# Optimization experiments

Hardware: AMD Instinct MI355X
Metric: run time of the kernel (lower is better)

The kernel has to match this reference:

```python
import jax, jax.numpy as jnp
import numpy as np

N, E, D, H = 100000, 400000, 128, 128  # nodes, edges, feat dim, mlp hidden


def _ln(x, g, b, eps=1e-5):
    m = jnp.mean(x, axis=-1, keepdims=True)
    v = jnp.mean((x - m) ** 2, axis=-1, keepdims=True)
    return (x - m) * jax.lax.rsqrt(v + eps) * g + b


def _mlp(x, w0, b0, w1, b1, w2, b2):
    # Linear->ReLU->Linear->ReLU->Linear (last act = Identity)
    h = jax.nn.relu(x @ w0 + b0)
    h = jax.nn.relu(h @ w1 + b1)
    return h @ w2 + b2


def setup_inputs() -> dict:
    key = jax.random.key(0)
    ks = jax.random.split(key, 16)
    node_x = jax.random.normal(ks[0], (N, D), dtype=jnp.float32)
    edge_attr = jax.random.normal(ks[1], (E, D), dtype=jnp.float32)
    edge_index = jax.random.randint(ks[2], (2, E), 0, N, dtype=jnp.int32)

    def lin(k, fin, fout):
        kw, kb = jax.random.split(k)
        s = 1.0 / np.sqrt(fin)
        w = jax.random.uniform(kw, (fin, fout), jnp.float32, -s, s)
        b = jax.random.uniform(kb, (fout,), jnp.float32, -s, s)
        return w, b

    # message MLP: (3D) -> H -> H -> D, then LayerNorm(D)
    msg_w0, msg_b0 = lin(ks[3], 3 * D, H)
    msg_w1, msg_b1 = lin(ks[4], H, H)
    msg_w2, msg_b2 = lin(ks[5], H, D)
    # top-level update MLP: (D + D) -> H -> H -> D, then LayerNorm(D)
    upd_w0, upd_b0 = lin(ks[6], 2 * D, H)
    upd_w1, upd_b1 = lin(ks[7], H, H)
    upd_w2, upd_b2 = lin(ks[8], H, D)
    return {
        "node_x": node_x, "edge_attr": edge_attr, "edge_index": edge_index,
        "msg_w0": msg_w0, "msg_b0": msg_b0, "msg_w1": msg_w1, "msg_b1": msg_b1,
        "msg_w2": msg_w2, "msg_b2": msg_b2,
        "msg_g": jnp.ones((D,), jnp.float32), "msg_beta": jnp.zeros((D,), jnp.float32),
        "upd_w0": upd_w0, "upd_b0": upd_b0, "upd_w1": upd_w1, "upd_b1": upd_b1,
        "upd_w2": upd_w2, "upd_b2": upd_b2,
        "upd_g": jnp.ones((D,), jnp.float32), "upd_beta": jnp.zeros((D,), jnp.float32),
    }


def reference(node_x, edge_attr, edge_index,
              msg_w0, msg_b0, msg_w1, msg_b1, msg_w2, msg_b2, msg_g, msg_beta,
              upd_w0, upd_b0, upd_w1, upd_b1, upd_w2, upd_b2, upd_g, upd_beta):
    src, dst = edge_index[0], edge_index[1]
    # PyG default flow source_to_target: x_j = x[src], x_i = x[dst]
    x_i = node_x[dst]                       # [E, D]
    x_j = node_x[src]                       # [E, D]
    concat = jnp.concatenate([x_i, x_j, edge_attr], axis=1)  # [E, 3D]
    msg = _ln(_mlp(concat, msg_w0, msg_b0, msg_w1, msg_b1, msg_w2, msg_b2), msg_g, msg_beta)
    new_edge = edge_attr + msg              # edge_attr[:] += msg in original
    # scatter-add messages onto target nodes
    agg = jax.ops.segment_sum(new_edge, dst, num_segments=N)  # [N, D]
    concat2 = jnp.concatenate([node_x, agg], axis=1)          # [N, 2D]
    upd = _ln(_mlp(concat2, upd_w0, upd_b0, upd_w1, upd_b1, upd_w2, upd_b2), upd_g, upd_beta)
    return node_x + upd
```

## Files before the change

kernel.cpp:

```cpp
#include <hip/hip_runtime.h>

typedef __attribute__((ext_vector_type(4))) float f32x4;
typedef __attribute__((ext_vector_type(8))) __bf16 bf16x8;

constexpr int FD = 128;

typedef __attribute__((address_space(3))) unsigned int* lds_u32p;
typedef const __attribute__((address_space(1))) unsigned int* gbl_u32p;

__device__ __forceinline__ uint4 pack8(const float* v) {
  union { __bf16 h[8]; uint4 u; } cv;
#pragma unroll
  for (int q = 0; q < 8; ++q) cv.h[q] = (__bf16)v[q];
  return cv.u;
}
__device__ __forceinline__ unsigned int pack2(float a, float b) {
  union { __bf16 h[2]; unsigned int u; } cv;
  cv.h[0] = (__bf16)a; cv.h[1] = (__bf16)b;
  return cv.u;
}

__global__ void cvt_bf16(const float* __restrict__ x, unsigned short* __restrict__ o, int n8) {
  int i = blockIdx.x * 256 + threadIdx.x;
  if (i >= n8) return;
  const float* p = x + (size_t)i * 8;
  float v[8];
#pragma unroll
  for (int q = 0; q < 8; ++q) v[q] = p[q];
  *(uint4*)(o + (size_t)i * 8) = pack8(v);
}

__global__ void pack_weights(const float* __restrict__ mw0, const float* __restrict__ mw1,
                             const float* __restrict__ mw2, const float* __restrict__ uw0,
                             const float* __restrict__ uw1, const float* __restrict__ uw2,
                             unsigned short* __restrict__ wp) {
  int tid = blockIdx.x * 256 + threadIdx.x;
  const float* src; int base, K;
  if      (tid < 49152)  { src = mw0; base = 0;      K = 384; }
  else if (tid < 65536)  { src = mw1; base = 49152;  K = 128; }
  else if (tid < 81920)  { src = mw2; base = 65536;  K = 128; }
  else if (tid < 114688) { src = uw0; base = 81920;  K = 256; }
  else if (tid < 131072) { src = uw1; base = 114688; K = 128; }
  else                   { src = uw2; base = 131072; K = 128; }
  int i = tid - base;
  int k = i >> 7, n = i & 127;
  int KS = K >> 5;
  int dst = base + (((n >> 4) * KS + (k >> 5)) * 64 + ((k >> 3) & 3) * 16 + (n & 15)) * 8 + (k & 7);
  union { __bf16 h; unsigned short s; } cv; cv.h = (__bf16)src[i];
  wp[dst] = cv.s;
}


template<bool RELU>
__device__ __forceinline__ void store_frag(unsigned short* sDst, const f32x4* acc, float bias) {
#pragma unroll
  for (int m = 0; m < 4; ++m)
#pragma unroll
    for (int ri = 0; ri < 4; ++ri) {
      float v = acc[m][ri] + bias;
      if (RELU) v = fmaxf(v, 0.f);
      union { __bf16 h; unsigned short s; } cv; cv.h = (__bf16)v;
      sDst[m * 512 + ri * 32] = cv.s;
    }
}

__global__ __launch_bounds__(512, 6)
void in_edge_kernel(const float* __restrict__ node_x, const unsigned short* __restrict__ nxbf,
                    const float* __restrict__ edge_attr,
                    const int* __restrict__ eidx, const unsigned short* __restrict__ wp,
                    const float* __restrict__ b0p, const float* __restrict__ b1p,
                    const float* __restrict__ b2p, const float* __restrict__ gp,
                    const float* __restrict__ bep,
                    unsigned short* __restrict__ msg, int* __restrict__ head,
                    int* __restrict__ nxt, float* __restrict__ agg,
                    int use_sort, int E) {
  __shared__ unsigned short sBuf[3072 * 8];
  __shared__ int sSrc[64], sDst[64];
  __shared__ float sG[128], sB[128];

  const int t = threadIdx.x;
  const int e0 = blockIdx.x * 64;
  const int lane = t & 63, w = t >> 6;
  const int ln = lane & 15, g16 = lane >> 4;
  const int rdoff = ln * 32 + g16 * 8;
  const int stoff = (w >> 1) * 2048 + g16 * 128
                  + (((2 * w) + (ln >> 3)) & 3) * 8 + (ln & 7);

  bf16x8 b0[6];
#pragma unroll
  for (int ks = 0; ks < 6; ++ks)
    b0[ks] = *(const bf16x8*)(wp + (size_t)((w * 12 + ks) * 64 + lane) * 8);
  bf16x8 B1r[4];
#pragma unroll
  for (int ks = 0; ks < 4; ++ks)
    B1r[ks] = *(const bf16x8*)(wp + 49152 + (size_t)((w * 4 + ks) * 64 + lane) * 8);

  if (t < 64) {
    sSrc[t] = (e0 + t < E) ? eidx[e0 + t] : 0;
  } else if (t < 128) {
    int r = t - 64;
    int e = e0 + r;
    int d = (e < E) ? eidx[E + e] : 0;
    sDst[r] = d;
    if (use_sort && e < E) nxt[e] = atomicExch(&head[d], e);
  } else if (t < 256) {
    sG[t - 128] = gp[t - 128];
  } else if (t < 384) {
    sB[t - 256] = bep[t - 256];
  }
  __syncthreads();

  if (nxbf) {
#pragma unroll
    for (int i = 0; i < 4; ++i) {
      int g = w * 4 + i;
      int tile = g >> 4;
      int ks = (g >> 2) & 3, m = g & 3;
      int row = m * 16 + (lane >> 2);
      int idx = tile ? sSrc[row] : sDst[row];
      const unsigned short* gp2 = nxbf + (size_t)idx * FD + ks * 32 + (lane & 3) * 8;
      lds_u32p lp = (lds_u32p)&sBuf[tile * 8192 + (size_t)(ks * 4 + m) * 512];
      __builtin_amdgcn_global_load_lds((gbl_u32p)gp2, lp, 16, 0, 0);
    }
  } else {
#pragma unroll
    for (int it = 0; it < 16; ++it) {
      const int type = it >> 3;
      int row = ((it & 7) << 3) + w;
      float2 v = {0.f, 0.f};
      if (e0 + row < E) {
        const float* sp = (type == 0) ? node_x + (size_t)sDst[row] * FD
                                      : node_x + (size_t)sSrc[row] * FD;
        v = *(const float2*)(sp + lane * 2);
      }
      int c = (((type * 4 + (lane >> 4)) * 4 + (row >> 4)) * 64
               + (row & 15) * 4 + ((lane >> 2) & 3)) * 8 + (lane & 3) * 2;
      *(unsigned int*)&sBuf[c] = pack2(v.x, v.y);
    }
  }
#pragma unroll
  for (int it = 0; it < 8; ++it) {
    int row = it * 8 + w;
    float2 v = {0.f, 0.f};
    if (e0 + row < E) v = *(const float2*)(edge_attr + (size_t)(e0 + row) * FD + lane * 2);
    int c = 16384 + (((lane >> 4) * 4 + (row >> 4)) * 64
                     + (row & 15) * 4 + ((lane >> 2) & 3)) * 8 + (lane & 3) * 2;
    *(unsigned int*)&sBuf[c] = pack2(v.x, v.y);
  }
  __syncthreads();

  const int col = w * 16 + ln;
  const float b0v = b0p[col], b1v = b1p[col], b2v = b2p[col];

  f32x4 acc[4];
#pragma unroll
  for (int m = 0; m < 4; ++m) acc[m] = (f32x4){0.f, 0.f, 0.f, 0.f};

#pragma unroll
  for (int ks = 0; ks < 12; ++ks) {
    bf16x8 bb = b0[ks % 6];
    if (ks + 6 < 12)
      b0[ks % 6] = *(const bf16x8*)(wp + (size_t)((w * 12 + ks + 6) * 64 + lane) * 8);
#pragma unroll
    for (int m = 0; m < 4; ++m) {
      bf16x8 a = *(const bf16x8*)&sBuf[(ks * 4 + m) * 512 + rdoff];
      acc[m] = __builtin_amdgcn_mfma_f32_16x16x32_bf16(a, bb, acc[m], 0, 0, 0);
    }
  }
  bf16x8 B2r[4];
#pragma unroll
  for (int ks = 0; ks < 4; ++ks)
    B2r[ks] = *(const bf16x8*)(wp + 65536 + (size_t)((w * 4 + ks) * 64 + lane) * 8);

  __syncthreads();
  store_frag<true>(sBuf + stoff, acc, b0v);
  __syncthreads();

#pragma unroll
  for (int m = 0; m < 4; ++m) acc[m] = (f32x4){0.f, 0.f, 0.f, 0.f};
#pragma unroll
  for (int ks = 0; ks < 4; ++ks)
#pragma unroll
    for (int m = 0; m < 4; ++m) {
      bf16x8 a = *(const bf16x8*)&sBuf[(ks * 4 + m) * 512 + rdoff];
      acc[m] = __builtin_amdgcn_mfma_f32_16x16x32_bf16(a, B1r[ks], acc[m], 0, 0, 0);
    }
  store_frag<true>(sBuf + 8192 + stoff, acc, b1v);
  __syncthreads();

#pragma unroll
  for (int m = 0; m < 4; ++m) acc[m] = (f32x4){0.f, 0.f, 0.f, 0.f};
#pragma unroll
  for (int ks = 0; ks < 4; ++ks)
#pragma unroll
    for (int m = 0; m < 4; ++m) {
      bf16x8 a = *(const bf16x8*)&sBuf[8192 + (ks * 4 + m) * 512 + rdoff];
      acc[m] = __builtin_amdgcn_mfma_f32_16x16x32_bf16(a, B2r[ks], acc[m], 0, 0, 0);
    }
  store_frag<false>(sBuf + stoff, acc, b2v);
  __syncthreads();

  {
    int row = t >> 3, j = t & 7;
    int a0 = (((j >> 1) * 4 + (row >> 4)) * 64 + (row & 15) * 4 + 2 * (j & 1)) * 8;
    bf16x8 v0 = *(const bf16x8*)&sBuf[a0];
    bf16x8 v1 = *(const bf16x8*)&sBuf[a0 + 8];
    float s1 = 0.f, s2 = 0.f;
#pragma unroll
    for (int q = 0; q < 8; ++q) {
      float a = (float)v0[q], b = (float)v1[q];
      s1 += a + b; s2 += a * a + b * b;
    }
#pragma unroll
    for (int m = 1; m < 8; m <<= 1) {
      s1 += __shfl_xor(s1, m, 64);
      s2 += __shfl_xor(s2, m, 64);
    }
    float mean = s1 * (1.f / 128.f);
    float var  = s2 * (1.f / 128.f) - mean * mean;
    float rstd = rsqrtf(fmaxf(var, 0.f) + 1e-5f);

    int e = e0 + row;
    if (e < E) {
      bf16x8 ea0 = *(const bf16x8*)&sBuf[a0 + 16384];
      bf16x8 ea1 = *(const bf16x8*)&sBuf[a0 + 16384 + 8];
      float val[16];
#pragma unroll
      for (int q = 0; q < 8; ++q) {
        val[q]     = ((float)v0[q] - mean) * rstd * sG[j * 16 + q]     + sB[j * 16 + q]     + (float)ea0[q];
        val[8 + q] = ((float)v1[q] - mean) * rstd * sG[j * 16 + 8 + q] + sB[j * 16 + 8 + q] + (float)ea1[q];
      }
      if (use_sort) {
        uint4* dst = (uint4*)(msg + (size_t)e * FD + j * 16);
        dst[0] = pack8(val);
        dst[1] = pack8(val + 8);
      } else {
        float* ap = agg + (size_t)sDst[row] * FD + j * 16;
#pragma unroll
        for (int q = 0; q < 16; ++q) atomicAdd(ap + q, val[q]);
      }
    }
  }
}

__global__ __launch_bounds__(512, 8)
void in_node_kernel(const float* __restrict__ node_x, const unsigned short* __restrict__ nxbf,
                    const unsigned short* __restrict__ msg, const int* __restrict__ head,
                    const int* __restrict__ nxt, const float* __restrict__ agg,
                    const unsigned short* __restrict__ wp,
                    const float* __restrict__ b0p, const float* __restrict__ b1p,
                    const float* __restrict__ b2p, const float* __restrict__ gp,
                    const float* __restrict__ bep, float* __restrict__ out,
                    int use_sort, int N) {
  __shared__ unsigned short sBuf[2048 * 8];
  __shared__ float sG[128], sB[128];

  const int t = threadIdx.x;
  const int r0 = blockIdx.x * 64;
  const int lane = t & 63, w = t >> 6;
  const int ln = lane & 15, g16 = lane >> 4;
  const int col = w * 16 + ln;
  const int rdoff = ln * 32 + g16 * 8;
  const int stoff = (w >> 1) * 2048 + g16 * 128
                  + (((2 * w) + (ln >> 3)) & 3) * 8 + (ln & 7);

  bf16x8 b0[4];
#pragma unroll
  for (int ks = 0; ks < 4; ++ks)
    b0[ks] = *(const bf16x8*)(wp + 81920 + (size_t)((w * 8 + ks) * 64 + lane) * 8);

  if (t < 128)      sG[t] = gp[t];
  else if (t < 256) sB[t - 128] = bep[t - 128];

  if (nxbf) {
#pragma unroll
    for (int i = 0; i < 2; ++i) {
      int g = w * 2 + i;
      int ks = g >> 2, m = g & 3;
      int row = m * 16 + (lane >> 2);
      const unsigned short* gp2 = nxbf + (size_t)(r0 + row) * FD + ks * 32 + (lane & 3) * 8;
      lds_u32p lp = (lds_u32p)&sBuf[(size_t)(ks * 4 + m) * 512];
      __builtin_amdgcn_global_load_lds((gbl_u32p)gp2, lp, 16, 0, 0);
    }
  } else {
#pragma unroll
    for (int it = 0; it < 8; ++it) {
      int row = (it << 3) + w;
      int r = r0 + row;
      float2 v = {0.f, 0.f};
      if (r < N) v = *(const float2*)(node_x + (size_t)r * FD + lane * 2);
      int c = (((lane >> 4) * 4 + (row >> 4)) * 64
               + (row & 15) * 4 + ((lane >> 2) & 3)) * 8 + (lane & 3) * 2;
      *(unsigned int*)&sBuf[c] = pack2(v.x, v.y);
    }
  }

  {
    int row = t >> 3, j = t & 7;
    int node = r0 + row;
    float a[16];
#pragma unroll
    for (int q = 0; q < 16; ++q) a[q] = 0.f;
    if (node < N) {
      if (use_sort) {
        int e = head[node];
        while (e >= 0) {
          int ne = nxt[e];
          bf16x8 m0 = *(const bf16x8*)(msg + (size_t)e * FD + j * 16);
          bf16x8 m1 = *(const bf16x8*)(msg + (size_t)e * FD + j * 16 + 8);
#pragma unroll
          for (int q = 0; q < 8; ++q) { a[q] += (float)m0[q]; a[8 + q] += (float)m1[q]; }
          e = ne;
        }
      } else {
        const float* ap = agg + (size_t)node * FD + j * 16;
#pragma unroll
        for (int q4 = 0; q4 < 4; ++q4) {
          f32x4 u = *(const f32x4*)(ap + q4 * 4);
#pragma unroll
          for (int q = 0; q < 4; ++q) a[q4 * 4 + q] = u[q];
        }
      }
    }
    int c = 8192 + (((j >> 1) * 4 + (row >> 4)) * 64 + (row & 15) * 4 + 2 * (j & 1)) * 8;
    *(uint4*)&sBuf[c] = pack8(a);
    *(uint4*)&sBuf[c + 8] = pack8(a + 8);
  }
  __syncthreads();

  const float b0v = b0p[col], b1v = b1p[col], b2v = b2p[col];

  f32x4 acc[4];
#pragma unroll
  for (int m = 0; m < 4; ++m) acc[m] = (f32x4){0.f, 0.f, 0.f, 0.f};

#pragma unroll
  for (int ks = 0; ks < 8; ++ks) {
    bf16x8 bb = b0[ks % 4];
    if (ks + 4 < 8)
      b0[ks % 4] = *(const bf16x8*)(wp + 81920 + (size_t)((w * 8 + ks + 4) * 64 + lane) * 8);
#pragma unroll
    for (int m = 0; m < 4; ++m) {
      bf16x8 a = *(const bf16x8*)&sBuf[(ks * 4 + m) * 512 + rdoff];
      acc[m] = __builtin_amdgcn_mfma_f32_16x16x32_bf16(a, bb, acc[m], 0, 0, 0);
    }
  }
  bf16x8 B1r[4];
#pragma unroll
  for (int ks = 0; ks < 4; ++ks)
    B1r[ks] = *(const bf16x8*)(wp + 114688 + (size_t)((w * 4 + ks) * 64 + lane) * 8);

  __syncthreads();
  store_frag<true>(sBuf + stoff, acc, b0v);
  __syncthreads();

#pragma unroll
  for (int m = 0; m < 4; ++m) acc[m] = (f32x4){0.f, 0.f, 0.f, 0.f};
#pragma unroll
  for (int ks = 0; ks < 4; ++ks)
#pragma unroll
    for (int m = 0; m < 4; ++m) {
      bf16x8 a = *(const bf16x8*)&sBuf[(ks * 4 + m) * 512 + rdoff];
      acc[m] = __builtin_amdgcn_mfma_f32_16x16x32_bf16(a, B1r[ks], acc[m], 0, 0, 0);
    }
  bf16x8 B2r[4];
#pragma unroll
  for (int ks = 0; ks < 4; ++ks)
    B2r[ks] = *(const bf16x8*)(wp + 131072 + (size_t)((w * 4 + ks) * 64 + lane) * 8);
  store_frag<true>(sBuf + 8192 + stoff, acc, b1v);
  __syncthreads();

#pragma unroll
  for (int m = 0; m < 4; ++m) acc[m] = (f32x4){0.f, 0.f, 0.f, 0.f};
#pragma unroll
  for (int ks = 0; ks < 4; ++ks)
#pragma unroll
    for (int m = 0; m < 4; ++m) {
      bf16x8 a = *(const bf16x8*)&sBuf[8192 + (ks * 4 + m) * 512 + rdoff];
      acc[m] = __builtin_amdgcn_mfma_f32_16x16x32_bf16(a, B2r[ks], acc[m], 0, 0, 0);
    }
  store_frag<false>(sBuf + stoff, acc, b2v);
  __syncthreads();

  {
    int row = t >> 3, j = t & 7;
    int a0 = (((j >> 1) * 4 + (row >> 4)) * 64 + (row & 15) * 4 + 2 * (j & 1)) * 8;
    bf16x8 v0 = *(const bf16x8*)&sBuf[a0];
    bf16x8 v1 = *(const bf16x8*)&sBuf[a0 + 8];
    float s1 = 0.f, s2 = 0.f;
#pragma unroll
    for (int q = 0; q < 8; ++q) {
      float a = (float)v0[q], b = (float)v1[q];
      s1 += a + b; s2 += a * a + b * b;
    }
#pragma unroll
    for (int m = 1; m < 8; m <<= 1) {
      s1 += __shfl_xor(s1, m, 64);
      s2 += __shfl_xor(s2, m, 64);
    }
    float mean = s1 * (1.f / 128.f);
    float var  = s2 * (1.f / 128.f) - mean * mean;
    float rstd = rsqrtf(fmaxf(var, 0.f) + 1e-5f);

    int node = r0 + row;
    if (node < N) {
      float o[16];
#pragma unroll
      for (int q = 0; q < 8; ++q) {
        o[q]     = ((float)v0[q] - mean) * rstd * sG[j * 16 + q]     + sB[j * 16 + q];
        o[8 + q] = ((float)v1[q] - mean) * rstd * sG[j * 16 + 8 + q] + sB[j * 16 + 8 + q];
      }
      const float* xr = node_x + (size_t)node * FD + j * 16;
      float* orow = out + (size_t)node * FD + j * 16;
#pragma unroll
      for (int q4 = 0; q4 < 4; ++q4) {
        f32x4 x = *(const f32x4*)(xr + q4 * 4);
        f32x4 wv;
#pragma unroll
        for (int q = 0; q < 4; ++q) wv[q] = o[q4 * 4 + q] + x[q];
        *(f32x4*)(orow + q4 * 4) = wv;
      }
    }
  }
}

extern "C" void kernel_launch(void* const* d_in, const int* in_sizes, int n_in,
                              void* d_out, int out_size, void* d_ws, size_t ws_size,
                              hipStream_t stream) {
  const float* node_x    = (const float*)d_in[0];
  const float* edge_attr = (const float*)d_in[1];
  const int*   eidx      = (const int*)d_in[2];
  const int N = in_sizes[0] / FD;
  const int E = in_sizes[1] / FD;

  char* ws = (char*)d_ws;
  auto aln = [](size_t x) { return (x + 255) & ~(size_t)255; };
  const size_t wpB   = aln(294912);
  const size_t nxbfB = aln((size_t)N * FD * 2 + 16384);
  const size_t headB = aln((size_t)N * 4);
  const size_t nxtB  = aln((size_t)E * 4);
  const size_t msgB  = (size_t)E * FD * 2;

  unsigned short* wp = (unsigned short*)ws;
  unsigned short* nxbf = nullptr;
  int* head = nullptr; int* nxt = nullptr;
  unsigned short* msg = nullptr; float* agg = nullptr;
  int use_sort = 0;

  if (ws_size >= wpB + nxbfB + headB + nxtB + msgB) {
    use_sort = 1;
    nxbf = (unsigned short*)(ws + wpB);
    head = (int*)(ws + wpB + nxbfB);
    nxt  = (int*)(ws + wpB + nxbfB + headB);
    msg  = (unsigned short*)(ws + wpB + nxbfB + headB + nxtB);
  } else if (ws_size >= wpB + headB + nxtB + msgB) {
    use_sort = 1;
    head = (int*)(ws + wpB);
    nxt  = (int*)(ws + wpB + headB);
    msg  = (unsigned short*)(ws + wpB + headB + nxtB);
  } else {
    agg = (float*)(ws + wpB);
  }

  if (use_sort) (void)hipMemsetAsync(head, 0xFF, (size_t)N * 4, stream);
  else          (void)hipMemsetAsync(agg, 0, (size_t)N * FD * sizeof(float), stream);

  pack_weights<<<576, 256, 0, stream>>>(
      (const float*)d_in[3], (const float*)d_in[5], (const float*)d_in[7],
      (const float*)d_in[11], (const float*)d_in[13], (const float*)d_in[15], wp);
  if (nxbf) cvt_bf16<<<(N * FD / 8 + 255) / 256, 256, 0, stream>>>(node_x, nxbf, N * FD / 8);
  in_edge_kernel<<<(E + 63) / 64, 512, 0, stream>>>(
      node_x, nxbf, edge_attr, eidx, wp,
      (const float*)d_in[4], (const float*)d_in[6], (const float*)d_in[8],
      (const float*)d_in[9], (const float*)d_in[10],
      msg, head, nxt, agg, use_sort, E);
  in_node_kernel<<<(N + 63) / 64, 512, 0, stream>>>(
      node_x, nxbf, msg, head, nxt, agg, wp,
      (const float*)d_in[12], (const float*)d_in[14], (const float*)d_in[16],
      (const float*)d_in[17], (const float*)d_in[18], (float*)d_out, use_sort, N);
}
```

Baseline: 240.1 us.

## Make edge kernel persistent and prefetch next tile's gathers during MLP

Turns the edge-message kernel into a grid-stride persistent kernel capped at 768 blocks when the bf16 node copy and sorted path are in use. While the current tile runs its later MLP stages, it issues async global-to-LDS gathers for the next tile's dst/src rows and reloads edge_attr, reusing freed LDS regions through a rotated buffer assignment. The aim is to hide gather latency and cut per-block launch and weight-reload overhead. The cost is extra barriers, tighter LDS reuse that risks data races, and less parallelism from the capped grid.

```diff
diff --git a/kernel.cpp b/kernel.cpp
--- a/kernel.cpp
+++ b/kernel.cpp
@@ -75,33 +75,33 @@
                     int* __restrict__ nxt, float* __restrict__ agg,
                     int use_sort, int E) {
   __shared__ unsigned short sBuf[3072 * 8];
-  __shared__ int sSrc[64], sDst[64];
+  __shared__ int sSrc[2][64], sDst[2][64];
   __shared__ float sG[128], sB[128];
 
   const int t = threadIdx.x;
-  const int e0 = blockIdx.x * 64;
   const int lane = t & 63, w = t >> 6;
   const int ln = lane & 15, g16 = lane >> 4;
   const int rdoff = ln * 32 + g16 * 8;
   const int stoff = (w >> 1) * 2048 + g16 * 128
                   + (((2 * w) + (ln >> 3)) & 3) * 8 + (ln & 7);
-
-  bf16x8 b0[6];
+  const int eStart = blockIdx.x * 64;
+  const int stride = gridDim.x * 64;
+
+  bf16x8 b0[6], B1r[4];
 #pragma unroll
   for (int ks = 0; ks < 6; ++ks)
     b0[ks] = *(const bf16x8*)(wp + (size_t)((w * 12 + ks) * 64 + lane) * 8);
-  bf16x8 B1r[4];
 #pragma unroll
   for (int ks = 0; ks < 4; ++ks)
     B1r[ks] = *(const bf16x8*)(wp + 49152 + (size_t)((w * 4 + ks) * 64 + lane) * 8);
 
   if (t < 64) {
-    sSrc[t] = (e0 + t < E) ? eidx[e0 + t] : 0;
+    sSrc[0][t] = (eStart + t < E) ? eidx[eStart + t] : 0;
   } else if (t < 128) {
     int r = t - 64;
-    int e = e0 + r;
+    int e = eStart + r;
     int d = (e < E) ? eidx[E + e] : 0;
-    sDst[r] = d;
+    sDst[0][r] = d;
     if (use_sort && e < E) nxt[e] = atomicExch(&head[d], e);
   } else if (t < 256) {
     sG[t - 128] = gp[t - 128];
@@ -110,134 +110,196 @@
   }
   __syncthreads();
 
-  if (nxbf) {
-#pragma unroll
-    for (int i = 0; i < 4; ++i) {
-      int g = w * 4 + i;
-      int tile = g >> 4;
-      int ks = (g >> 2) & 3, m = g & 3;
-      int row = m * 16 + (lane >> 2);
-      int idx = tile ? sSrc[row] : sDst[row];
-      const unsigned short* gp2 = nxbf + (size_t)idx * FD + ks * 32 + (lane & 3) * 8;
-      lds_u32p lp = (lds_u32p)&sBuf[tile * 8192 + (size_t)(ks * 4 + m) * 512];
-      __builtin_amdgcn_global_load_lds((gbl_u32p)gp2, lp, 16, 0, 0);
-    }
-  } else {
-#pragma unroll
-    for (int it = 0; it < 16; ++it) {
-      const int type = it >> 3;
-      int row = ((it & 7) << 3) + w;
+  if (eStart < E) {
+    if (nxbf) {
+#pragma unroll
+      for (int i = 0; i < 4; ++i) {
+        int g = w * 4 + i;
+        int tile = g >> 4;
+        int ks = (g >> 2) & 3, m = g & 3;
+        int row = m * 16 + (lane >> 2);
+        int idx = tile ? sSrc[0][row] : sDst[0][row];
+        const unsigned short* gp2 = nxbf + (size_t)idx * FD + ks * 32 + (lane & 3) * 8;
+        lds_u32p lp = (lds_u32p)&sBuf[tile * 8192 + (size_t)(ks * 4 + m) * 512];
+        __builtin_amdgcn_global_load_lds((gbl_u32p)gp2, lp, 16, 0, 0);
+      }
+    } else {
+#pragma unroll
+      for (int it = 0; it < 16; ++it) {
+        const int type = it >> 3;
+        int row = ((it & 7) << 3) + w;
+        float2 v = {0.f, 0.f};
+        if (eStart + row < E) {
+          const float* sp = (type == 0) ? node_x + (size_t)sDst[0][row] * FD
+                                        : node_x + (size_t)sSrc[0][row] * FD;
+          v = *(const float2*)(sp + lane * 2);
+        }
+        int c = (((type * 4 + (lane >> 4)) * 4 + (row >> 4)) * 64
+                 + (row & 15) * 4 + ((lane >> 2) & 3)) * 8 + (lane & 3) * 2;
+        *(unsigned int*)&sBuf[c] = pack2(v.x, v.y);
+      }
+    }
+#pragma unroll
+    for (int it = 0; it < 8; ++it) {
+      int row = it * 8 + w;
       float2 v = {0.f, 0.f};
-      if (e0 + row < E) {
-        const float* sp = (type == 0) ? node_x + (size_t)sDst[row] * FD
-                                      : node_x + (size_t)sSrc[row] * FD;
-        v = *(const float2*)(sp + lane * 2);
-      }
-      int c = (((type * 4 + (lane >> 4)) * 4 + (row >> 4)) * 64
-               + (row & 15) * 4 + ((lane >> 2) & 3)) * 8 + (lane & 3) * 2;
+      if (eStart + row < E) v = *(const float2*)(edge_attr + (size_t)(eStart + row) * FD + lane * 2);
+      int c = 16384 + (((lane >> 4) * 4 + (row >> 4)) * 64
+                       + (row & 15) * 4 + ((lane >> 2) & 3)) * 8 + (lane & 3) * 2;
       *(unsigned int*)&sBuf[c] = pack2(v.x, v.y);
     }
   }
-#pragma unroll
-  for (int it = 0; it < 8; ++it) {
-    int row = it * 8 + w;
-    float2 v = {0.f, 0.f};
-    if (e0 + row < E) v = *(const float2*)(edge_attr + (size_t)(e0 + row) * FD + lane * 2);
-    int c = 16384 + (((lane >> 4) * 4 + (row >> 4)) * 64
-                     + (row & 15) * 4 + ((lane >> 2) & 3)) * 8 + (lane & 3) * 2;
-    *(unsigned int*)&sBuf[c] = pack2(v.x, v.y);
-  }
-  __syncthreads();
 
   const int col = w * 16 + ln;
   const float b0v = b0p[col], b1v = b1p[col], b2v = b2p[col];
 
-  f32x4 acc[4];
-#pragma unroll
-  for (int m = 0; m < 4; ++m) acc[m] = (f32x4){0.f, 0.f, 0.f, 0.f};
-
-#pragma unroll
-  for (int ks = 0; ks < 12; ++ks) {
-    bf16x8 bb = b0[ks % 6];
-    if (ks + 6 < 12)
-      b0[ks % 6] = *(const bf16x8*)(wp + (size_t)((w * 12 + ks + 6) * 64 + lane) * 8);
-#pragma unroll
-    for (int m = 0; m < 4; ++m) {
-      bf16x8 a = *(const bf16x8*)&sBuf[(ks * 4 + m) * 512 + rdoff];
-      acc[m] = __builtin_amdgcn_mfma_f32_16x16x32_bf16(a, bb, acc[m], 0, 0, 0);
-    }
-  }
-  bf16x8 B2r[4];
-#pragma unroll
-  for (int ks = 0; ks < 4; ++ks)
-    B2r[ks] = *(const bf16x8*)(wp + 65536 + (size_t)((w * 4 + ks) * 64 + lane) * 8);
-
-  __syncthreads();
-  store_frag<true>(sBuf + stoff, acc, b0v);
-  __syncthreads();
-
-#pragma unroll
-  for (int m = 0; m < 4; ++m) acc[m] = (f32x4){0.f, 0.f, 0.f, 0.f};
-#pragma unroll
-  for (int ks = 0; ks < 4; ++ks)
-#pragma unroll
-    for (int m = 0; m < 4; ++m) {
-      bf16x8 a = *(const bf16x8*)&sBuf[(ks * 4 + m) * 512 + rdoff];
-      acc[m] = __builtin_amdgcn_mfma_f32_16x16x32_bf16(a, B1r[ks], acc[m], 0, 0, 0);
-    }
-  store_frag<true>(sBuf + 8192 + stoff, acc, b1v);
-  __syncthreads();
-
-#pragma unroll
-  for (int m = 0; m < 4; ++m) acc[m] = (f32x4){0.f, 0.f, 0.f, 0.f};
-#pragma unroll
-  for (int ks = 0; ks < 4; ++ks)
-#pragma unroll
-    for (int m = 0; m < 4; ++m) {
-      bf16x8 a = *(const bf16x8*)&sBuf[8192 + (ks * 4 + m) * 512 + rdoff];
-      acc[m] = __builtin_amdgcn_mfma_f32_16x16x32_bf16(a, B2r[ks], acc[m], 0, 0, 0);
-    }
-  store_frag<false>(sBuf + stoff, acc, b2v);
-  __syncthreads();
-
-  {
-    int row = t >> 3, j = t & 7;
-    int a0 = (((j >> 1) * 4 + (row >> 4)) * 64 + (row & 15) * 4 + 2 * (j & 1)) * 8;
-    bf16x8 v0 = *(const bf16x8*)&sBuf[a0];
-    bf16x8 v1 = *(const bf16x8*)&sBuf[a0 + 8];
-    float s1 = 0.f, s2 = 0.f;
-#pragma unroll
-    for (int q = 0; q < 8; ++q) {
-      float a = (float)v0[q], b = (float)v1[q];
-      s1 += a + b; s2 += a * a + b * b;
-    }
-#pragma unroll
-    for (int m = 1; m < 8; m <<= 1) {
-      s1 += __shfl_xor(s1, m, 64);
-      s2 += __shfl_xor(s2, m, 64);
-    }
-    float mean = s1 * (1.f / 128.f);
-    float var  = s2 * (1.f / 128.f) - mean * mean;
-    float rstd = rsqrtf(fmaxf(var, 0.f) + 1e-5f);
-
-    int e = e0 + row;
-    if (e < E) {
-      bf16x8 ea0 = *(const bf16x8*)&sBuf[a0 + 16384];
-      bf16x8 ea1 = *(const bf16x8*)&sBuf[a0 + 16384 + 8];
-      float val[16];
+  int cb = 0;
+  for (int e0 = eStart; e0 < E; e0 += stride, cb ^= 1) {
+    const bool hasNext = nxbf && (e0 + stride < E);
+    __syncthreads();
+
+    f32x4 acc[4];
+#pragma unroll
+    for (int m = 0; m < 4; ++m) acc[m] = (f32x4){0.f, 0.f, 0.f, 0.f};
+
+#pragma unroll
+    for (int ks = 0; ks < 12; ++ks) {
+      bf16x8 bb = b0[ks % 6];
+      if (ks + 6 < 12)
+        b0[ks % 6] = *(const bf16x8*)(wp + (size_t)((w * 12 + ks + 6) * 64 + lane) * 8);
+#pragma unroll
+      for (int m = 0; m < 4; ++m) {
+        bf16x8 a = *(const bf16x8*)&sBuf[(ks * 4 + m) * 512 + rdoff];
+        acc[m] = __builtin_amdgcn_mfma_f32_16x16x32_bf16(a, bb, acc[m], 0, 0, 0);
+      }
+    }
+    bf16x8 B2r[4];
+#pragma unroll
+    for (int ks = 0; ks < 4; ++ks)
+      B2r[ks] = *(const bf16x8*)(wp + 65536 + (size_t)((w * 4 + ks) * 64 + lane) * 8);
+
+    __syncthreads();
+    store_frag<true>(sBuf + 8192 + stoff, acc, b0v);
+    if (hasNext) {
+      int eN = e0 + stride;
+      if (t < 64) {
+        sSrc[cb ^ 1][t] = (eN + t < E) ? eidx[eN + t] : 0;
+      } else if (t < 128) {
+        int r = t - 64;
+        int e = eN + r;
+        int d = (e < E) ? eidx[E + e] : 0;
+        sDst[cb ^ 1][r] = d;
+        if (use_sort && e < E) nxt[e] = atomicExch(&head[d], e);
+      }
+    }
+    __syncthreads();
+
+#pragma unroll
+    for (int m = 0; m < 4; ++m) acc[m] = (f32x4){0.f, 0.f, 0.f, 0.f};
+#pragma unroll
+    for (int ks = 0; ks < 4; ++ks)
+#pragma unroll
+      for (int m = 0; m < 4; ++m) {
+        bf16x8 a = *(const bf16x8*)&sBuf[8192 + (ks * 4 + m) * 512 + rdoff];
+        acc[m] = __builtin_amdgcn_mfma_f32_16x16x32_bf16(a, B1r[ks], acc[m], 0, 0, 0);
+      }
+    store_frag<true>(sBuf + stoff, acc, b1v);
+    __syncthreads();
+
+#pragma unroll
+    for (int m = 0; m < 4; ++m) acc[m] = (f32x4){0.f, 0.f, 0.f, 0.f};
+#pragma unroll
+    for (int ks = 0; ks < 4; ++ks)
+#pragma unroll
+      for (int m = 0; m < 4; ++m) {
+        bf16x8 a = *(const bf16x8*)&sBuf[(ks * 4 + m) * 512 + rdoff];
+        acc[m] = __builtin_amdgcn_mfma_f32_16x16x32_bf16(a, B2r[ks], acc[m], 0, 0, 0);
+      }
+    store_frag<false>(sBuf + 8192 + stoff, acc, b2v);
+    __syncthreads();
+
+    if (hasNext) {
+#pragma unroll
+      for (int i = 0; i < 2; ++i) {
+        int g = w * 2 + i;
+        int ks = g >> 2, m = g & 3;
+        int row = m * 16 + (lane >> 2);
+        int idx = sDst[cb ^ 1][row];
+        const unsigned short* gp2 = nxbf + (size_t)idx * FD + ks * 32 + (lane & 3) * 8;
+        lds_u32p lp = (lds_u32p)&sBuf[(size_t)(ks * 4 + m) * 512];
+        __builtin_amdgcn_global_load_lds((gbl_u32p)gp2, lp, 16, 0, 0);
+      }
+    }
+
+    {
+      int row = t >> 3, j = t & 7;
+      int a0 = (((j >> 1) * 4 + (row >> 4)) * 64 + (row & 15) * 4 + 2 * (j & 1)) * 8;
+      bf16x8 v0 = *(const bf16x8*)&sBuf[8192 + a0];
+      bf16x8 v1 = *(const bf16x8*)&sBuf[8192 + a0 + 8];
+      float s1 = 0.f, s2 = 0.f;
 #pragma unroll
       for (int q = 0; q < 8; ++q) {
-        val[q]     = ((float)v0[q] - mean) * rstd * sG[j * 16 + q]     + sB[j * 16 + q]     + (float)ea0[q];
-        val[8 + q] = ((float)v1[q] - mean) * rstd * sG[j * 16 + 8 + q] + sB[j * 16 + 8 + q] + (float)ea1[q];
-      }
-      if (use_sort) {
-        uint4* dst = (uint4*)(msg + (size_t)e * FD + j * 16);
-        dst[0] = pack8(val);
-        dst[1] = pack8(val + 8);
-      } else {
-        float* ap = agg + (size_t)sDst[row] * FD + j * 16;
-#pragma unroll
-        for (int q = 0; q < 16; ++q) atomicAdd(ap + q, val[q]);
+        float a = (float)v0[q], b = (float)v1[q];
+        s1 += a + b; s2 += a * a + b * b;
+      }
+#pragma unroll
+      for (int m = 1; m < 8; m <<= 1) {
+        s1 += __shfl_xor(s1, m, 64);
+        s2 += __shfl_xor(s2, m, 64);
+      }
+      float mean = s1 * (1.f / 128.f);
+      float var  = s2 * (1.f / 128.f) - mean * mean;
+      float rstd = rsqrtf(fmaxf(var, 0.f) + 1e-5f);
+
+      int e = e0 + row;
+      if (e < E) {
+        bf16x8 ea0 = *(const bf16x8*)&sBuf[16384 + a0];
+        bf16x8 ea1 = *(const bf16x8*)&sBuf[16384 + a0 + 8];
+        float val[16];
+#pragma unroll
+        for (int q = 0; q < 8; ++q) {
+          val[q]     = ((float)v0[q] - mean) * rstd * sG[j * 16 + q]     + sB[j * 16 + q]     + (float)ea0[q];
+          val[8 + q] = ((float)v1[q] - mean) * rstd * sG[j * 16 + 8 + q] + sB[j * 16 + 8 + q] + (float)ea1[q];
+        }
+        if (use_sort) {
+          uint4* dst = (uint4*)(msg + (size_t)e * FD + j * 16);
+          dst[0] = pack8(val);
+          dst[1] = pack8(val + 8);
+        } else {
+          float* ap = agg + (size_t)sDst[cb][row] * FD + j * 16;
+#pragma unroll
+          for (int q = 0; q < 16; ++q) atomicAdd(ap + q, val[q]);
+        }
+      }
+    }
+
+    if (hasNext) {
+#pragma unroll
+      for (int ks = 0; ks < 6; ++ks)
+        b0[ks] = *(const bf16x8*)(wp + (size_t)((w * 12 + ks) * 64 + lane) * 8);
+    }
+    __syncthreads();
+
+    if (hasNext) {
+#pragma unroll
+      for (int i = 0; i < 2; ++i) {
+        int g = w * 2 + i;
+        int ks = g >> 2, m = g & 3;
+        int row = m * 16 + (lane >> 2);
+        int idx = sSrc[cb ^ 1][row];
+        const unsigned short* gp2 = nxbf + (size_t)idx * FD + ks * 32 + (lane & 3) * 8;
+        lds_u32p lp = (lds_u32p)&sBuf[8192 + (size_t)(ks * 4 + m) * 512];
+        __builtin_amdgcn_global_load_lds((gbl_u32p)gp2, lp, 16, 0, 0);
+      }
+      int eN = e0 + stride;
+#pragma unroll
+      for (int it = 0; it < 8; ++it) {
+        int row = it * 8 + w;
+        float2 v = {0.f, 0.f};
+        if (eN + row < E) v = *(const float2*)(edge_attr + (size_t)(eN + row) * FD + lane * 2);
+        int c = 16384 + (((lane >> 4) * 4 + (row >> 4)) * 64
+                         + (row & 15) * 4 + ((lane >> 2) & 3)) * 8 + (lane & 3) * 2;
+        *(unsigned int*)&sBuf[c] = pack2(v.x, v.y);
       }
     }
   }
@@ -469,7 +531,10 @@
       (const float*)d_in[3], (const float*)d_in[5], (const float*)d_in[7],
       (const float*)d_in[11], (const float*)d_in[13], (const float*)d_in[15], wp);
   if (nxbf) cvt_bf16<<<(N * FD / 8 + 255) / 256, 256, 0, stream>>>(node_x, nxbf, N * FD / 8);
-  in_edge_kernel<<<(E + 63) / 64, 512, 0, stream>>>(
+
+  int nt = (E + 63) / 64;
+  int egrid = (nxbf && use_sort) ? (nt < 768 ? nt : 768) : nt;
+  in_edge_kernel<<<egrid, 512, 0, stream>>>(
       node_x, nxbf, edge_attr, eidx, wp,
       (const float*)d_in[4], (const float*)d_in[6], (const float*)d_in[8],
       (const float*)d_in[9], (const float*)d_in[10],
```

New measurement: 385.2 us. 60.5% more time.
